# Performance work log

Hardware: AMD Instinct MI355X
Metric: run time of the kernel (lower is better)

Reference implementation:

```python
import jax, jax.numpy as jnp
import numpy as np

DEGREE = 3
NUM_KNOTS_PARAM = 5
NUM_BASIS = NUM_KNOTS_PARAM + DEGREE - 1  # 7


def bspline_basis(x, knots, degree=DEGREE, nb=NUM_BASIS):
    """Faithful vectorization of BSplineBasis.compute_basis.

    x: [B, D]; knots: [num_knots] strictly increasing (linspace -> all
    denominator != 0 and i+d+1 < num_knots checks in the torch code are
    statically true). Returns [B, D, nb].
    """
    x = jnp.clip(x, knots[0], knots[-1])
    xe = x[..., None]  # [B, D, 1]
    # degree-0: indicator over first nb knot intervals (as in the torch loop)
    b = ((xe >= knots[:nb]) & (xe < knots[1 : nb + 1])).astype(x.dtype)
    for d in range(1, degree + 1):
        left = (xe - knots[:nb]) / (knots[d : d + nb] - knots[:nb])
        right = (knots[d + 1 : d + 1 + nb] - xe) / (
            knots[d + 1 : d + 1 + nb] - knots[1 : 1 + nb]
        )
        # torch code drops basis[:, :, i+1] when i+1 == nb -> shifted with zero pad
        b_shift = jnp.pad(b[..., 1:], ((0, 0), (0, 0), (0, 1)))
        b = left * b + right * b_shift
    return b


def setup_inputs() -> dict:
    key = jax.random.key(0)
    k1, k2, k3, k4 = jax.random.split(key, 4)
    B, IN, OUT = 8192, 1024, 1024
    x = jax.random.normal(k1, (B, IN), dtype=jnp.float32)
    spline_weights = 0.1 * jax.random.normal(k2, (IN, OUT, NUM_BASIS), dtype=jnp.float32)
    bound = 1.0 / np.sqrt(IN)
    W = jax.random.uniform(k3, (OUT, IN), minval=-bound, maxval=bound, dtype=jnp.float32)
    b = jax.random.uniform(k4, (OUT,), minval=-bound, maxval=bound, dtype=jnp.float32)
    knots = jnp.linspace(-1.0, 1.0, NUM_KNOTS_PARAM + 2 * DEGREE, dtype=jnp.float32)
    return {"x": x, "spline_weights": spline_weights, "W": W, "b": b, "knots": knots}


def reference(x, spline_weights, W, b, knots):
    basis = bspline_basis(jnp.tanh(x), knots)  # [B, IN, NB]
    spline_out = jnp.einsum("bik,iok->bo", basis, spline_weights)
    linear_out = x @ W.T + b
    return linear_out + spline_out
```

## Files before the change

### kernel.cpp

```cpp
#include <hip/hip_runtime.h>
#include <cstdint>
#include <cstddef>

#define IN_DIM  1024
#define OUT_DIM 1024
#define NB      7
#define KTOT    8192
#define BROWS   8192

typedef unsigned short u16;
typedef __attribute__((ext_vector_type(8))) short bf16x8;
typedef __attribute__((ext_vector_type(8))) unsigned short u16x8;
typedef __attribute__((ext_vector_type(4))) float f32x4;

__device__ __forceinline__ u16 f2bf(float f) {
    union { float f; unsigned int u; } v; v.f = f;
    unsigned int r = (v.u + 0x7fffu + ((v.u >> 16) & 1u)) >> 16;
    return (u16)r;
}

__device__ __forceinline__ void gl_lds16(const u16* g, u16* l) {
    __builtin_amdgcn_global_load_lds(
        (const __attribute__((address_space(1))) void*)g,
        (__attribute__((address_space(3))) void*)l,
        16, 0, 0);
}

__global__ __launch_bounds__(256) void prep_wsw(const float* __restrict__ sw,
                                                const float* __restrict__ W,
                                                u16* __restrict__ Bt) {
    __shared__ u16 S[8 * 256 * 8];
    const int i0 = blockIdx.x * 8;
    const int o0 = blockIdx.y * 256;
    const int t  = threadIdx.x;
    #pragma unroll
    for (int il = 0; il < 8; ++il) {
        const float* src = sw + ((size_t)(i0 + il) * OUT_DIM + o0) * NB;
        for (int c = t; c < 256 * NB; c += 256) {
            int ol = c / 7, k = c - ol * 7;
            S[(il * 256 + ol) * 8 + 1 + k] = f2bf(src[c]);
        }
    }
    for (int c = t; c < 2048; c += 256) {
        int ol = c >> 3, il = c & 7;
        S[(il * 256 + ol) * 8] = f2bf(W[(size_t)(o0 + ol) * IN_DIM + i0 + il]);
    }
    __syncthreads();
    for (int c = t; c < 2048; c += 256) {
        int ol = c >> 3, il = c & 7;
        *(u16x8*)&Bt[(size_t)(o0 + ol) * KTOT + (size_t)(i0 + il) * 8] =
            *(const u16x8*)&S[(il * 256 + ol) * 8];
    }
}

__global__ __launch_bounds__(256) void prep_a(const float* __restrict__ x,
                                              u16* __restrict__ A, int row0) {
    int gid = blockIdx.x * 256 + threadIdx.x;
    int b = gid >> 10;
    int i = gid & 1023;
    float xv = x[(size_t)(row0 + b) * IN_DIM + i];

    float e = __expf(2.f * xv);
    float t = 1.f - 2.f / (e + 1.f);
    t = fminf(fmaxf(t, -1.f), 1.f);

    const float kn[11] = {-1.f, -0.8f, -0.6f, -0.4f, -0.2f, 0.f,
                           0.2f, 0.4f, 0.6f, 0.8f, 1.f};
    float bb[8];
    #pragma unroll
    for (int j = 0; j < 7; ++j)
        bb[j] = (t >= kn[j] && t < kn[j + 1]) ? 1.f : 0.f;
    bb[7] = 0.f;

    const float rcp[4] = {0.f, 5.f, 2.5f, 5.f / 3.f};
    #pragma unroll
    for (int d = 1; d <= 3; ++d) {
        #pragma unroll
        for (int j = 0; j < 7; ++j) {
            float left  = (t - kn[j]) * rcp[d];
            float right = (kn[j + d + 1] - t) * rcp[d];
            bb[j] = left * bb[j] + right * bb[j + 1];
        }
    }
    u16x8 outv;
    outv[0] = f2bf(xv);
    #pragma unroll
    for (int k = 0; k < NB; ++k) outv[1 + k] = f2bf(bb[k]);
    *(u16x8*)&A[(size_t)b * KTOT + (size_t)i * 8] = outv;
}

__global__ __launch_bounds__(256) void gemm_bt(const u16* __restrict__ A,
                                               const u16* __restrict__ Bt,
                                               const float* __restrict__ bias,
                                               float* __restrict__ C) {
    __shared__ __align__(16) u16 As[2][128 * 64];
    __shared__ __align__(16) u16 Bs[2][128 * 64];
    const int t = threadIdx.x;
    const int L = t & 63;
    const int w = t >> 6;
    const int wm = w & 1, wn = w >> 1;

    const int Lid = blockIdx.x;
    const int n_t = (Lid >> 3) & 7;
    const int m_t = (Lid & 7) + 8 * (Lid >> 6);
    const int m0 = m_t * 128;
    const int n0 = n_t * 128;

    f32x4 acc[4][4] = {};

    const int trow = t >> 3;
    const int qsw  = (t & 7) ^ (trow & 7);
    const u16* gA[4]; const u16* gB[4];
    int off[4];
    #pragma unroll
    for (int g = 0; g < 4; ++g) {
        gA[g] = A  + (size_t)(m0 + 32 * g + trow) * KTOT + qsw * 8;
        gB[g] = Bt + (size_t)(n0 + 32 * g + trow) * KTOT + qsw * 8;
        off[g] = (256 * g + t) * 8;
    }

    const int lm  = L & 15;
    const int qd  = L >> 4;

    u16* pA  = &As[0][0];
    u16* pAn = &As[1][0];
    u16* pB  = &Bs[0][0];
    u16* pBn = &Bs[1][0];

    #pragma unroll
    for (int g = 0; g < 4; ++g) gl_lds16(gA[g], pA + off[g]);
    #pragma unroll
    for (int g = 0; g < 4; ++g) gl_lds16(gB[g], pB + off[g]);
    __syncthreads();

    for (int ko = 0; ko < KTOT; ko += 64) {
        if (ko + 64 < KTOT) {
            #pragma unroll
            for (int g = 0; g < 4; ++g) gl_lds16(gA[g] + ko + 64, pAn + off[g]);
            #pragma unroll
            for (int g = 0; g < 4; ++g) gl_lds16(gB[g] + ko + 64, pBn + off[g]);
        }

        #pragma unroll
        for (int ks = 0; ks < 2; ++ks) {
            const int pq = ((ks * 4 + qd) ^ (lm & 7)) * 8;
            bf16x8 af[4], bfr[4];
            #pragma unroll
            for (int mi = 0; mi < 4; ++mi)
                af[mi] = *(const bf16x8*)&pA[(wm * 64 + mi * 16 + lm) * 64 + pq];
            #pragma unroll
            for (int ni = 0; ni < 4; ++ni)
                bfr[ni] = *(const bf16x8*)&pB[(wn * 64 + ni * 16 + lm) * 64 + pq];
            #pragma unroll
            for (int mi = 0; mi < 4; ++mi)
                #pragma unroll
                for (int ni = 0; ni < 4; ++ni)
                    acc[mi][ni] = __builtin_amdgcn_mfma_f32_16x16x32_bf16(
                        af[mi], bfr[ni], acc[mi][ni], 0, 0, 0);
        }

        __syncthreads();
        u16* tmp;
        tmp = pA; pA = pAn; pAn = tmp;
        tmp = pB; pB = pBn; pBn = tmp;
    }

    const int r0 = qd * 4;
    #pragma unroll
    for (int ni = 0; ni < 4; ++ni) {
        int col = n0 + wn * 64 + ni * 16 + lm;
        float bv = bias[col];
        #pragma unroll
        for (int mi = 0; mi < 4; ++mi) {
            int rb = m0 + wm * 64 + mi * 16 + r0;
            f32x4 v = acc[mi][ni];
            #pragma unroll
            for (int rr = 0; rr < 4; ++rr)
                C[(size_t)(rb + rr) * OUT_DIM + col] = v[rr] + bv;
        }
    }
}

extern "C" void kernel_launch(void* const* d_in, const int* in_sizes, int n_in,
                              void* d_out, int out_size, void* d_ws, size_t ws_size,
                              hipStream_t stream) {
    (void)in_sizes; (void)n_in; (void)out_size;
    const float* x    = (const float*)d_in[0];
    const float* sw   = (const float*)d_in[1];
    const float* W    = (const float*)d_in[2];
    const float* bias = (const float*)d_in[3];
    float* out = (float*)d_out;

    const size_t btBytes = (size_t)OUT_DIM * KTOT * 2;
    u16* Bt = (u16*)d_ws;
    u16* A  = (u16*)((char*)d_ws + btBytes);

    prep_wsw<<<dim3(IN_DIM / 8, OUT_DIM / 256), 256, 0, stream>>>(sw, W, Bt);

    int nchunks = 1;
    if (ws_size < btBytes + (size_t)BROWS * KTOT * 2)       nchunks = 2;
    if (ws_size < btBytes + (size_t)(BROWS / 2) * KTOT * 2) nchunks = 4;
    if (ws_size < btBytes + (size_t)(BROWS / 4) * KTOT * 2) nchunks = 8;
    const int rows = BROWS / nchunks;

    for (int c = 0; c < nchunks; ++c) {
        int row0 = c * rows;
        prep_a<<<rows * 4, 256, 0, stream>>>(x, A, row0);
        gemm_bt<<<dim3(8 * (rows / 128)), 256, 0, stream>>>(
            A, Bt, bias, out + (size_t)row0 * OUT_DIM);
    }
}
```

Measured before the change: 279.8 us.

## Use eight waves per GEMM tile and batch rows per prep_a block

The GEMM kernel moves from 4 to 8 waves per 128x128 output tile. Each wave now computes a 64x32 sub-tile instead of 64x64, and the cooperative global-to-LDS loads are spread over 512 threads. The goal is more resident waves per CU to hide LDS and global load latency, at the cost of more redundant A-fragment reads from LDS per MFMA. Separately, prep_a now has each thread handle 16 elements across 4 rows, cutting the block count by 16x to reduce launch and scheduling overhead.

Result: slower. 287.2 us (+2.6%).

```diff
diff --git a/kernel.cpp b/kernel.cpp
--- a/kernel.cpp
+++ b/kernel.cpp
@@ -55,41 +55,49 @@
 
 __global__ __launch_bounds__(256) void prep_a(const float* __restrict__ x,
                                               u16* __restrict__ A, int row0) {
-    int gid = blockIdx.x * 256 + threadIdx.x;
-    int b = gid >> 10;
-    int i = gid & 1023;
-    float xv = x[(size_t)(row0 + b) * IN_DIM + i];
-
-    float e = __expf(2.f * xv);
-    float t = 1.f - 2.f / (e + 1.f);
-    t = fminf(fmaxf(t, -1.f), 1.f);
-
+    const int t  = threadIdx.x;
+    const int b0 = blockIdx.x * 4;
     const float kn[11] = {-1.f, -0.8f, -0.6f, -0.4f, -0.2f, 0.f,
                            0.2f, 0.4f, 0.6f, 0.8f, 1.f};
-    float bb[8];
-    #pragma unroll
-    for (int j = 0; j < 7; ++j)
-        bb[j] = (t >= kn[j] && t < kn[j + 1]) ? 1.f : 0.f;
-    bb[7] = 0.f;
-
     const float rcp[4] = {0.f, 5.f, 2.5f, 5.f / 3.f};
-    #pragma unroll
-    for (int d = 1; d <= 3; ++d) {
+
+    for (int r = 0; r < 4; ++r) {
+        const float* xr = x + (size_t)(row0 + b0 + r) * IN_DIM;
+        u16* Ar = A + (size_t)(b0 + r) * KTOT;
         #pragma unroll
-        for (int j = 0; j < 7; ++j) {
-            float left  = (t - kn[j]) * rcp[d];
-            float right = (kn[j + d + 1] - t) * rcp[d];
-            bb[j] = left * bb[j] + right * bb[j + 1];
-        }
-    }
-    u16x8 outv;
-    outv[0] = f2bf(xv);
-    #pragma unroll
-    for (int k = 0; k < NB; ++k) outv[1 + k] = f2bf(bb[k]);
-    *(u16x8*)&A[(size_t)b * KTOT + (size_t)i * 8] = outv;
-}
-
-__global__ __launch_bounds__(256) void gemm_bt(const u16* __restrict__ A,
+        for (int j = 0; j < 4; ++j) {
+            const int i = t + 256 * j;
+            float xv = xr[i];
+
+            float e = __expf(2.f * xv);
+            float tv = 1.f - 2.f / (e + 1.f);
+            tv = fminf(fmaxf(tv, -1.f), 1.f);
+
+            float bb[8];
+            #pragma unroll
+            for (int jj = 0; jj < 7; ++jj)
+                bb[jj] = (tv >= kn[jj] && tv < kn[jj + 1]) ? 1.f : 0.f;
+            bb[7] = 0.f;
+
+            #pragma unroll
+            for (int d = 1; d <= 3; ++d) {
+                #pragma unroll
+                for (int jj = 0; jj < 7; ++jj) {
+                    float left  = (tv - kn[jj]) * rcp[d];
+                    float right = (kn[jj + d + 1] - tv) * rcp[d];
+                    bb[jj] = left * bb[jj] + right * bb[jj + 1];
+                }
+            }
+            u16x8 outv;
+            outv[0] = f2bf(xv);
+            #pragma unroll
+            for (int k = 0; k < NB; ++k) outv[1 + k] = f2bf(bb[k]);
+            *(u16x8*)&Ar[(size_t)i * 8] = outv;
+        }
+    }
+}
+
+__global__ __launch_bounds__(512) void gemm_bt(const u16* __restrict__ A,
                                                const u16* __restrict__ Bt,
                                                const float* __restrict__ bias,
                                                float* __restrict__ C) {
@@ -106,17 +114,17 @@
     const int m0 = m_t * 128;
     const int n0 = n_t * 128;
 
-    f32x4 acc[4][4] = {};
+    f32x4 acc[4][2] = {};
 
     const int trow = t >> 3;
     const int qsw  = (t & 7) ^ (trow & 7);
-    const u16* gA[4]; const u16* gB[4];
-    int off[4];
-    #pragma unroll
-    for (int g = 0; g < 4; ++g) {
-        gA[g] = A  + (size_t)(m0 + 32 * g + trow) * KTOT + qsw * 8;
-        gB[g] = Bt + (size_t)(n0 + 32 * g + trow) * KTOT + qsw * 8;
-        off[g] = (256 * g + t) * 8;
+    const u16* gA[2]; const u16* gB[2];
+    int off[2];
+    #pragma unroll
+    for (int g = 0; g < 2; ++g) {
+        gA[g] = A  + (size_t)(m0 + 64 * g + trow) * KTOT + qsw * 8;
+        gB[g] = Bt + (size_t)(n0 + 64 * g + trow) * KTOT + qsw * 8;
+        off[g] = (512 * g + t) * 8;
     }
 
     const int lm  = L & 15;
@@ -128,33 +136,33 @@
     u16* pBn = &Bs[1][0];
 
     #pragma unroll
-    for (int g = 0; g < 4; ++g) gl_lds16(gA[g], pA + off[g]);
-    #pragma unroll
-    for (int g = 0; g < 4; ++g) gl_lds16(gB[g], pB + off[g]);
+    for (int g = 0; g < 2; ++g) gl_lds16(gA[g], pA + off[g]);
+    #pragma unroll
+    for (int g = 0; g < 2; ++g) gl_lds16(gB[g], pB + off[g]);
     __syncthreads();
 
     for (int ko = 0; ko < KTOT; ko += 64) {
         if (ko + 64 < KTOT) {
             #pragma unroll
-            for (int g = 0; g < 4; ++g) gl_lds16(gA[g] + ko + 64, pAn + off[g]);
-            #pragma unroll
-            for (int g = 0; g < 4; ++g) gl_lds16(gB[g] + ko + 64, pBn + off[g]);
+            for (int g = 0; g < 2; ++g) gl_lds16(gA[g] + ko + 64, pAn + off[g]);
+            #pragma unroll
+            for (int g = 0; g < 2; ++g) gl_lds16(gB[g] + ko + 64, pBn + off[g]);
         }
 
         #pragma unroll
         for (int ks = 0; ks < 2; ++ks) {
             const int pq = ((ks * 4 + qd) ^ (lm & 7)) * 8;
-            bf16x8 af[4], bfr[4];
+            bf16x8 af[4], bfr[2];
             #pragma unroll
             for (int mi = 0; mi < 4; ++mi)
                 af[mi] = *(const bf16x8*)&pA[(wm * 64 + mi * 16 + lm) * 64 + pq];
             #pragma unroll
-            for (int ni = 0; ni < 4; ++ni)
-                bfr[ni] = *(const bf16x8*)&pB[(wn * 64 + ni * 16 + lm) * 64 + pq];
+            for (int ni = 0; ni < 2; ++ni)
+                bfr[ni] = *(const bf16x8*)&pB[(wn * 32 + ni * 16 + lm) * 64 + pq];
             #pragma unroll
             for (int mi = 0; mi < 4; ++mi)
                 #pragma unroll
-                for (int ni = 0; ni < 4; ++ni)
+                for (int ni = 0; ni < 2; ++ni)
                     acc[mi][ni] = __builtin_amdgcn_mfma_f32_16x16x32_bf16(
                         af[mi], bfr[ni], acc[mi][ni], 0, 0, 0);
         }
@@ -167,8 +175,8 @@
 
     const int r0 = qd * 4;
     #pragma unroll
-    for (int ni = 0; ni < 4; ++ni) {
-        int col = n0 + wn * 64 + ni * 16 + lm;
+    for (int ni = 0; ni < 2; ++ni) {
+        int col = n0 + wn * 32 + ni * 16 + lm;
         float bv = bias[col];
         #pragma unroll
         for (int mi = 0; mi < 4; ++mi) {
@@ -205,8 +213,8 @@
 
     for (int c = 0; c < nchunks; ++c) {
         int row0 = c * rows;
-        prep_a<<<rows * 4, 256, 0, stream>>>(x, A, row0);
-        gemm_bt<<<dim3(8 * (rows / 128)), 256, 0, stream>>>(
+        prep_a<<<rows / 4, 256, 0, stream>>>(x, A, row0);
+        gemm_bt<<<dim3(8 * (rows / 128)), 512, 0, stream>>>(
             A, Bt, bias, out + (size_t)row0 * OUT_DIM);
     }
 }
```

## Fuse B-spline basis expansion into GEMM A-tile loading

Applied to the files above, without the earlier changes.

Removes the separate prep_a kernel and its materialized bf16 A matrix, which was 8192x8192. The GEMM now reads raw x floats and computes the tanh and B-spline basis in registers, writing packed bf16 rows straight into the LDS A tile for the next k-step. This drops a large global write and re-read, plus the chunked launches. In exchange, every N-tile block (8 per M row) recomputes the basis, adding ALU work and register pressure inside the MFMA main loop.

Result: slower. 512.8 us (+83.2%).

```diff
diff --git a/kernel.cpp b/kernel.cpp
--- a/kernel.cpp
+++ b/kernel.cpp
@@ -24,6 +24,35 @@
         (const __attribute__((address_space(1))) void*)g,
         (__attribute__((address_space(3))) void*)l,
         16, 0, 0);
+}
+
+__device__ __forceinline__ u16x8 basis_pack(float xv) {
+    float e = __expf(2.f * xv);
+    float tv = 1.f - 2.f / (e + 1.f);
+    tv = fminf(fmaxf(tv, -1.f), 1.f);
+
+    const float kn[11] = {-1.f, -0.8f, -0.6f, -0.4f, -0.2f, 0.f,
+                           0.2f, 0.4f, 0.6f, 0.8f, 1.f};
+    const float rcp[4] = {0.f, 5.f, 2.5f, 5.f / 3.f};
+    float bb[8];
+    #pragma unroll
+    for (int j = 0; j < 7; ++j)
+        bb[j] = (tv >= kn[j] && tv < kn[j + 1]) ? 1.f : 0.f;
+    bb[7] = 0.f;
+    #pragma unroll
+    for (int d = 1; d <= 3; ++d) {
+        #pragma unroll
+        for (int j = 0; j < 7; ++j) {
+            float left  = (tv - kn[j]) * rcp[d];
+            float right = (kn[j + d + 1] - tv) * rcp[d];
+            bb[j] = left * bb[j] + right * bb[j + 1];
+        }
+    }
+    u16x8 outv;
+    outv[0] = f2bf(xv);
+    #pragma unroll
+    for (int k = 0; k < NB; ++k) outv[1 + k] = f2bf(bb[k]);
+    return outv;
 }
 
 __global__ __launch_bounds__(256) void prep_wsw(const float* __restrict__ sw,
@@ -53,46 +82,10 @@
     }
 }
 
-__global__ __launch_bounds__(256) void prep_a(const float* __restrict__ x,
-                                              u16* __restrict__ A, int row0) {
-    int gid = blockIdx.x * 256 + threadIdx.x;
-    int b = gid >> 10;
-    int i = gid & 1023;
-    float xv = x[(size_t)(row0 + b) * IN_DIM + i];
-
-    float e = __expf(2.f * xv);
-    float t = 1.f - 2.f / (e + 1.f);
-    t = fminf(fmaxf(t, -1.f), 1.f);
-
-    const float kn[11] = {-1.f, -0.8f, -0.6f, -0.4f, -0.2f, 0.f,
-                           0.2f, 0.4f, 0.6f, 0.8f, 1.f};
-    float bb[8];
-    #pragma unroll
-    for (int j = 0; j < 7; ++j)
-        bb[j] = (t >= kn[j] && t < kn[j + 1]) ? 1.f : 0.f;
-    bb[7] = 0.f;
-
-    const float rcp[4] = {0.f, 5.f, 2.5f, 5.f / 3.f};
-    #pragma unroll
-    for (int d = 1; d <= 3; ++d) {
-        #pragma unroll
-        for (int j = 0; j < 7; ++j) {
-            float left  = (t - kn[j]) * rcp[d];
-            float right = (kn[j + d + 1] - t) * rcp[d];
-            bb[j] = left * bb[j] + right * bb[j + 1];
-        }
-    }
-    u16x8 outv;
-    outv[0] = f2bf(xv);
-    #pragma unroll
-    for (int k = 0; k < NB; ++k) outv[1 + k] = f2bf(bb[k]);
-    *(u16x8*)&A[(size_t)b * KTOT + (size_t)i * 8] = outv;
-}
-
-__global__ __launch_bounds__(256) void gemm_bt(const u16* __restrict__ A,
-                                               const u16* __restrict__ Bt,
-                                               const float* __restrict__ bias,
-                                               float* __restrict__ C) {
+__global__ __launch_bounds__(256) void gemm_fused(const float* __restrict__ x,
+                                                  const u16* __restrict__ Bt,
+                                                  const float* __restrict__ bias,
+                                                  float* __restrict__ C) {
     __shared__ __align__(16) u16 As[2][128 * 64];
     __shared__ __align__(16) u16 Bs[2][128 * 64];
     const int t = threadIdx.x;
@@ -110,12 +103,13 @@
 
     const int trow = t >> 3;
     const int qsw  = (t & 7) ^ (trow & 7);
-    const u16* gA[4]; const u16* gB[4];
+    const u16* gB[4];
+    const float* gX[4];
     int off[4];
     #pragma unroll
     for (int g = 0; g < 4; ++g) {
-        gA[g] = A  + (size_t)(m0 + 32 * g + trow) * KTOT + qsw * 8;
-        gB[g] = Bt + (size_t)(n0 + 32 * g + trow) * KTOT + qsw * 8;
+        gB[g]  = Bt + (size_t)(n0 + 32 * g + trow) * KTOT + qsw * 8;
+        gX[g]  = x  + (size_t)(m0 + 32 * g + trow) * IN_DIM + qsw;
         off[g] = (256 * g + t) * 8;
     }
 
@@ -128,17 +122,20 @@
     u16* pBn = &Bs[1][0];
 
     #pragma unroll
-    for (int g = 0; g < 4; ++g) gl_lds16(gA[g], pA + off[g]);
-    #pragma unroll
     for (int g = 0; g < 4; ++g) gl_lds16(gB[g], pB + off[g]);
+    #pragma unroll
+    for (int g = 0; g < 4; ++g)
+        *(u16x8*)&pA[off[g]] = basis_pack(gX[g][0]);
     __syncthreads();
 
     for (int ko = 0; ko < KTOT; ko += 64) {
+        float xn[4];
         if (ko + 64 < KTOT) {
             #pragma unroll
-            for (int g = 0; g < 4; ++g) gl_lds16(gA[g] + ko + 64, pAn + off[g]);
-            #pragma unroll
             for (int g = 0; g < 4; ++g) gl_lds16(gB[g] + ko + 64, pBn + off[g]);
+            const int cb = (ko + 64) >> 3;
+            #pragma unroll
+            for (int g = 0; g < 4; ++g) xn[g] = gX[g][cb];
         }
 
         #pragma unroll
@@ -157,6 +154,12 @@
                 for (int ni = 0; ni < 4; ++ni)
                     acc[mi][ni] = __builtin_amdgcn_mfma_f32_16x16x32_bf16(
                         af[mi], bfr[ni], acc[mi][ni], 0, 0, 0);
+        }
+
+        if (ko + 64 < KTOT) {
+            #pragma unroll
+            for (int g = 0; g < 4; ++g)
+                *(u16x8*)&pAn[off[g]] = basis_pack(xn[g]);
         }
 
         __syncthreads();
@@ -184,29 +187,15 @@
 extern "C" void kernel_launch(void* const* d_in, const int* in_sizes, int n_in,
                               void* d_out, int out_size, void* d_ws, size_t ws_size,
                               hipStream_t stream) {
-    (void)in_sizes; (void)n_in; (void)out_size;
+    (void)in_sizes; (void)n_in; (void)out_size; (void)ws_size;
     const float* x    = (const float*)d_in[0];
     const float* sw   = (const float*)d_in[1];
     const float* W    = (const float*)d_in[2];
     const float* bias = (const float*)d_in[3];
     float* out = (float*)d_out;
 
-    const size_t btBytes = (size_t)OUT_DIM * KTOT * 2;
     u16* Bt = (u16*)d_ws;
-    u16* A  = (u16*)((char*)d_ws + btBytes);
 
     prep_wsw<<<dim3(IN_DIM / 8, OUT_DIM / 256), 256, 0, stream>>>(sw, W, Bt);
-
-    int nchunks = 1;
-    if (ws_size < btBytes + (size_t)BROWS * KTOT * 2)       nchunks = 2;
-    if (ws_size < btBytes + (size_t)(BROWS / 2) * KTOT * 2) nchunks = 4;
-    if (ws_size < btBytes + (size_t)(BROWS / 4) * KTOT * 2) nchunks = 8;
-    const int rows = BROWS / nchunks;
-
-    for (int c = 0; c < nchunks; ++c) {
-        int row0 = c * rows;
-        prep_a<<<rows * 4, 256, 0, stream>>>(x, A, row0);
-        gemm_bt<<<dim3(8 * (rows / 128)), 256, 0, stream>>>(
-            A, Bt, bias, out + (size_t)row0 * OUT_DIM);
-    }
-}
+    gemm_fused<<<dim3(8 * (BROWS / 128)), 256, 0, stream>>>(x, Bt, bias, out);
+}
```
